# Performance work log

Hardware: AMD Instinct MI355X
Metric: run time of the kernel (lower is better)

## Reference

```python
import jax, jax.numpy as jnp
import numpy as np

B, N1, N2, H, LAT, MID = 16, 2048, 2048, 768, 128, 256


def setup_inputs() -> dict:
    key = jax.random.key(0)
    ks = jax.random.split(key, 20)
    def lin(k, n_in, n_out):
        s = 1.0 / np.sqrt(n_in)
        kw, kb = jax.random.split(k)
        W = jax.random.uniform(kw, (n_in, n_out), jnp.float32, -s, s)
        b = jax.random.uniform(kb, (n_out,), jnp.float32, -s, s)
        return W, b
    We1, be1 = lin(ks[0], H, MID)
    We2, be2 = lin(ks[1], MID, LAT)
    Wq, bq = lin(ks[2], LAT, LAT)
    Wk, bk = lin(ks[3], LAT, LAT)
    Wv, bv = lin(ks[4], LAT, LAT)
    Wd1, bd1 = lin(ks[5], LAT, MID)
    Wd2, bd2 = lin(ks[6], MID, H)
    main_feature = jax.random.normal(ks[7], (B, N1, H), jnp.float32)
    feature = jax.random.normal(ks[8], (B, N2, H), jnp.float32)
    return dict(main_feature=main_feature, feature=feature,
                We1=We1, be1=be1, We2=We2, be2=be2,
                Wq=Wq, bq=bq, Wk=Wk, bk=bk, Wv=Wv, bv=bv,
                Wd1=Wd1, bd1=bd1, Wd2=Wd2, bd2=bd2)


def reference(main_feature, feature, We1, be1, We2, be2, Wq, bq, Wk, bk, Wv, bv, Wd1, bd1, Wd2, bd2):
    def encode(x):
        h = jax.nn.relu(x @ We1 + be1)
        return jax.nn.relu(h @ We2 + be2)  # [B, N, LAT]

    def decode(x):
        h = jax.nn.relu(x @ Wd1 + bd1)
        return jax.nn.sigmoid(h @ Wd2 + bd2)  # [B, N, H]

    m = encode(main_feature)           # [B, N1, LAT]
    f = encode(feature)                # [B, N2, LAT]
    q = m @ Wq + bq                    # [B, N1, LAT]
    k = f @ Wk + bk                    # [B, N2, LAT]
    v = f @ Wv + bv                    # [B, N2, LAT]
    scores = jnp.einsum('bnd,bmd->bnm', q, k)   # unscaled, [B, N1, N2]
    probs = jax.nn.softmax(scores, axis=-1)
    attn = jnp.einsum('bnm,bmd->bnd', probs, v)  # [B, N1, LAT]
    return decode(attn)                # [B, N1, H]
```

## Files before the change

kernel.cpp:

```cpp
#include <hip/hip_runtime.h>
#include <stdint.h>

typedef unsigned short u16;
typedef __bf16 bf16x8 __attribute__((ext_vector_type(8)));
typedef float f32x4 __attribute__((ext_vector_type(4)));

#define MM   32768

__device__ __forceinline__ u16 f2bf(float f) {
    uint32_t u; __builtin_memcpy(&u, &f, 4);
    u += 0x7fffu + ((u >> 16) & 1u);
    return (u16)(u >> 16);
}

__device__ __forceinline__ void gl_lds16(const u16* g, u16* l) {
    __builtin_amdgcn_global_load_lds(
        (__attribute__((address_space(1))) void*)(g),
        (__attribute__((address_space(3))) void*)(l), 16, 0, 0);
}

__global__ void transpose_all(const float* __restrict__ We1, const float* __restrict__ We2,
                              const float* __restrict__ Wq,  const float* __restrict__ Wk,
                              const float* __restrict__ Wv,  const float* __restrict__ Wd1,
                              const float* __restrict__ Wd2, u16* __restrict__ wt) {
    int i = blockIdx.x * 256 + threadIdx.x;
    const float* src; int K, N, off;
    if      (i < 196608) { src = We1; K = 768; N = 256; off = i;          }
    else if (i < 229376) { src = We2; K = 256; N = 128; off = i - 196608; }
    else if (i < 245760) { src = Wq;  K = 128; N = 128; off = i - 229376; }
    else if (i < 262144) { src = Wk;  K = 128; N = 128; off = i - 245760; }
    else if (i < 278528) { src = Wv;  K = 128; N = 128; off = i - 262144; }
    else if (i < 311296) { src = Wd1; K = 128; N = 256; off = i - 278528; }
    else if (i < 507904) { src = Wd2; K = 256; N = 768; off = i - 311296; }
    else return;
    int n = off / K, k = off % K;
    wt[i] = f2bf(src[(size_t)k * N + n]);
}

template <int ACT, bool TRANS, bool A_F32, bool OUT_F32>
__global__ void gemm_bt(const void* __restrict__ Avp, const u16* __restrict__ Wt,
                        const float* __restrict__ bias, void* __restrict__ Cvp,
                        int M, int N, int K) {
    __shared__ u16 a_sh[128 * 64];
    __shared__ u16 b_sh[128 * 64];
    const int t = threadIdx.x;
    const int wave = t >> 6, lane = t & 63;
    const int lrow = lane & 15, quad = lane >> 4;
    const int wr = wave >> 1, wc = wave & 1;
    const int m0 = blockIdx.x * 128, n0 = blockIdx.y * 128;

    f32x4 acc[4][4];
#pragma unroll
    for (int i = 0; i < 4; i++)
#pragma unroll
        for (int j = 0; j < 4; j++) acc[i][j] = (f32x4){0.f, 0.f, 0.f, 0.f};

    for (int k0 = 0; k0 < K; k0 += 64) {
        if (A_F32) {
            const float* Af = (const float*)Avp;
#pragma unroll
            for (int it = 0; it < 8; it++) {
                int s = it * 256 + t;
                int row = s >> 4, kc = s & 15;
                float4 v = *(const float4*)(Af + (size_t)(m0 + row) * K + k0 + kc * 4);
                uint32_t p0 = (uint32_t)f2bf(v.x) | ((uint32_t)f2bf(v.y) << 16);
                uint32_t p1 = (uint32_t)f2bf(v.z) | ((uint32_t)f2bf(v.w) << 16);
                *(uint32_t*)&a_sh[row * 64 + kc * 4]     = p0;
                *(uint32_t*)&a_sh[row * 64 + kc * 4 + 2] = p1;
            }
        } else {
            const u16* Ab = (const u16*)Avp;
#pragma unroll
            for (int it = 0; it < 4; it++) {
                int s = it * 256 + t;
                gl_lds16(Ab + (size_t)(m0 + (s >> 3)) * K + k0 + (s & 7) * 8,
                         &a_sh[(it * 256 + wave * 64) * 8]);
            }
        }
#pragma unroll
        for (int it = 0; it < 4; it++) {
            int s = it * 256 + t;
            gl_lds16(Wt + (size_t)(n0 + (s >> 3)) * K + k0 + (s & 7) * 8,
                     &b_sh[(it * 256 + wave * 64) * 8]);
        }
        __syncthreads();
#pragma unroll
        for (int kk = 0; kk < 2; kk++) {
            bf16x8 af[4], bfv[4];
#pragma unroll
            for (int i = 0; i < 4; i++)
                af[i] = *(const bf16x8*)&a_sh[(wr * 64 + i * 16 + lrow) * 64 + kk * 32 + quad * 8];
#pragma unroll
            for (int j = 0; j < 4; j++)
                bfv[j] = *(const bf16x8*)&b_sh[(wc * 64 + j * 16 + lrow) * 64 + kk * 32 + quad * 8];
#pragma unroll
            for (int i = 0; i < 4; i++)
#pragma unroll
                for (int j = 0; j < 4; j++)
                    acc[i][j] = __builtin_amdgcn_mfma_f32_16x16x32_bf16(af[i], bfv[j], acc[i][j], 0, 0, 0);
        }
        __syncthreads();
    }

    float bv4[4];
#pragma unroll
    for (int j = 0; j < 4; j++) bv4[j] = bias[n0 + wc * 64 + j * 16 + lrow];

#pragma unroll
    for (int i = 0; i < 4; i++) {
#pragma unroll
        for (int j = 0; j < 4; j++) {
            const int col = n0 + wc * 64 + j * 16 + lrow;
            if (!TRANS) {
#pragma unroll
                for (int r = 0; r < 4; r++) {
                    float x = acc[i][j][r] + bv4[j];
                    if (ACT == 1) x = fmaxf(x, 0.f);
                    if (ACT == 2) x = 1.f / (1.f + __expf(-x));
                    const int row = m0 + wr * 64 + i * 16 + quad * 4 + r;
                    if (OUT_F32) ((float*)Cvp)[(size_t)row * N + col] = x;
                    else         ((u16*)Cvp)[(size_t)row * N + col] = f2bf(x);
                }
            } else {
                u16 vv[4];
#pragma unroll
                for (int r = 0; r < 4; r++) vv[r] = f2bf(acc[i][j][r] + bv4[j]);
                u16* Cb = (u16*)Cvp;
                size_t base = (size_t)(m0 >> 11) * ((size_t)N * 2048) + (size_t)col * 2048 +
                              (m0 & 2047) + wr * 64 + i * 16 + quad * 4;
                *(uint32_t*)&Cb[base]     = (uint32_t)vv[0] | ((uint32_t)vv[1] << 16);
                *(uint32_t*)&Cb[base + 2] = (uint32_t)vv[2] | ((uint32_t)vv[3] << 16);
            }
        }
    }
}

__global__ __launch_bounds__(256)
void flash_attn(const u16* __restrict__ Q, const u16* __restrict__ Kb,
                const u16* __restrict__ VT, u16* __restrict__ O) {
    __shared__ u16 k_sh[64 * 128];
    __shared__ u16 v_sh[128 * 64];
    __shared__ u16 qp_sh[64 * 128];

    const int t = threadIdx.x, wave = t >> 6, lane = t & 63;
    const int lrow = lane & 15, quad = lane >> 4;
    const int lsw = (lrow & 7) << 3;
    const int b = blockIdx.x >> 5, q0 = (blockIdx.x & 31) * 64;

    const u16* qg = Q + (size_t)(b * 2048 + q0) * 128;
#pragma unroll
    for (int it = 0; it < 4; it++) {
        int s = it * 256 + t;
        int srcSeg = s ^ ((s >> 4) & 7);
        gl_lds16(qg + (size_t)srcSeg * 8, &qp_sh[(it * 256 + wave * 64) * 8]);
    }
    __syncthreads();
    bf16x8 qf[4];
#pragma unroll
    for (int ks = 0; ks < 4; ks++)
        qf[ks] = *(const bf16x8*)&qp_sh[(((wave * 16 + lrow) * 128) + ks * 32 + quad * 8) ^ lsw];

    f32x4 o_acc[8];
#pragma unroll
    for (int ct = 0; ct < 8; ct++) o_acc[ct] = (f32x4){0.f, 0.f, 0.f, 0.f};
    float m_i[4] = {-1e30f, -1e30f, -1e30f, -1e30f};
    float l_i[4] = {0.f, 0.f, 0.f, 0.f};

    for (int tile = 0; tile < 32; tile++) {
        const u16* kg = Kb + (size_t)(b * 2048 + tile * 64) * 128;
        const u16* vg = VT + (size_t)b * 262144 + tile * 64;
#pragma unroll
        for (int it = 0; it < 4; it++) {
            int s = it * 256 + t;
            int srcSeg = s ^ ((s >> 4) & 7);
            gl_lds16(kg + (size_t)srcSeg * 8, &k_sh[(it * 256 + wave * 64) * 8]);
        }
#pragma unroll
        for (int it = 0; it < 4; it++) {
            int s = it * 256 + t;
            int row = s >> 3, c = (s & 7) ^ (row & 7);
            gl_lds16(vg + (size_t)row * 2048 + c * 8,
                     &v_sh[(it * 256 + wave * 64) * 8]);
        }
        __syncthreads();

        f32x4 s_acc[4];
        __builtin_amdgcn_s_setprio(1);
#pragma unroll
        for (int ct = 0; ct < 4; ct++) {
            f32x4 a = (f32x4){0.f, 0.f, 0.f, 0.f};
#pragma unroll
            for (int ks = 0; ks < 4; ks++) {
                bf16x8 kf = *(const bf16x8*)&k_sh[(((ct * 16 + lrow) * 128) + ks * 32 + quad * 8) ^ lsw];
                a = __builtin_amdgcn_mfma_f32_16x16x32_bf16(qf[ks], kf, a, 0, 0, 0);
            }
            s_acc[ct] = a;
        }
        __builtin_amdgcn_s_setprio(0);

        float mnew[4], alpha[4], ps[4];
#pragma unroll
        for (int r = 0; r < 4; r++) {
            float mx = s_acc[0][r];
#pragma unroll
            for (int ct = 1; ct < 4; ct++) mx = fmaxf(mx, s_acc[ct][r]);
#pragma unroll
            for (int d = 8; d >= 1; d >>= 1) mx = fmaxf(mx, __shfl_xor(mx, d, 64));
            mnew[r] = fmaxf(m_i[r], mx);
            alpha[r] = __expf(m_i[r] - mnew[r]);
            m_i[r] = mnew[r];
            ps[r] = 0.f;
        }
#pragma unroll
        for (int ct = 0; ct < 4; ct++)
#pragma unroll
            for (int r = 0; r < 4; r++) {
                float p = __expf(s_acc[ct][r] - mnew[r]);
                ps[r] += p;
                qp_sh[(((wave * 16 + quad * 4 + r) * 128) + ct * 16 + lrow) ^ (((quad * 4 + r) & 7) << 3)] = f2bf(p);
            }
#pragma unroll
        for (int r = 0; r < 4; r++) {
#pragma unroll
            for (int d = 8; d >= 1; d >>= 1) ps[r] += __shfl_xor(ps[r], d, 64);
            l_i[r] = l_i[r] * alpha[r] + ps[r];
        }
#pragma unroll
        for (int ct = 0; ct < 8; ct++)
#pragma unroll
            for (int r = 0; r < 4; r++) o_acc[ct][r] *= alpha[r];

        bf16x8 pf[2];
#pragma unroll
        for (int ks = 0; ks < 2; ks++)
            pf[ks] = *(const bf16x8*)&qp_sh[(((wave * 16 + lrow) * 128) + ks * 32 + quad * 8) ^ lsw];
        __builtin_amdgcn_s_setprio(1);
#pragma unroll
        for (int ct = 0; ct < 8; ct++)
#pragma unroll
            for (int ks = 0; ks < 2; ks++) {
                bf16x8 vf = *(const bf16x8*)&v_sh[(((ct * 16 + lrow) * 64) + ks * 32 + quad * 8) ^ lsw];
                o_acc[ct] = __builtin_amdgcn_mfma_f32_16x16x32_bf16(pf[ks], vf, o_acc[ct], 0, 0, 0);
            }
        __builtin_amdgcn_s_setprio(0);
        __syncthreads();
    }

    float inv_l[4];
#pragma unroll
    for (int r = 0; r < 4; r++) inv_l[r] = 1.f / l_i[r];
#pragma unroll
    for (int ct = 0; ct < 8; ct++)
#pragma unroll
        for (int r = 0; r < 4; r++) {
            const int row = b * 2048 + q0 + wave * 16 + quad * 4 + r;
            O[(size_t)row * 128 + ct * 16 + lrow] = f2bf(o_acc[ct][r] * inv_l[r]);
        }
}

extern "C" void kernel_launch(void* const* d_in, const int* in_sizes, int n_in,
                              void* d_out, int out_size, void* d_ws, size_t ws_size,
                              hipStream_t stream) {
    const float* mainf = (const float*)d_in[0];
    const float* feat  = (const float*)d_in[1];
    const float* We1 = (const float*)d_in[2];  const float* be1 = (const float*)d_in[3];
    const float* We2 = (const float*)d_in[4];  const float* be2 = (const float*)d_in[5];
    const float* Wq  = (const float*)d_in[6];  const float* bq  = (const float*)d_in[7];
    const float* Wk  = (const float*)d_in[8];  const float* bk  = (const float*)d_in[9];
    const float* Wv  = (const float*)d_in[10]; const float* bv  = (const float*)d_in[11];
    const float* Wd1 = (const float*)d_in[12]; const float* bd1 = (const float*)d_in[13];
    const float* Wd2 = (const float*)d_in[14]; const float* bd2 = (const float*)d_in[15];

    u16* ws = (u16*)d_ws;
    u16* wt = ws;
    u16* h1 = wt + 524288;
    u16* mf = h1 + 8388608;
    u16* qb = mf + 4194304;
    u16* kb = qb + 4194304;
    u16* vT = kb + 4194304;
    u16* wt_e1 = wt, *wt_e2 = wt + 196608, *wt_q = wt + 229376, *wt_k = wt + 245760,
       * wt_v = wt + 262144, *wt_d1 = wt + 278528, *wt_d2 = wt + 311296;

    transpose_all<<<1984, 256, 0, stream>>>(We1, We2, Wq, Wk, Wv, Wd1, Wd2, wt);

    gemm_bt<1, false, true,  false><<<dim3(256, 2), 256, 0, stream>>>(mainf, wt_e1, be1, h1, MM, 256, 768);
    gemm_bt<1, false, false, false><<<dim3(256, 1), 256, 0, stream>>>(h1,    wt_e2, be2, mf, MM, 128, 256);
    gemm_bt<0, false, false, false><<<dim3(256, 1), 256, 0, stream>>>(mf,    wt_q,  bq,  qb, MM, 128, 128);
    gemm_bt<1, false, true,  false><<<dim3(256, 2), 256, 0, stream>>>(feat, wt_e1, be1, h1, MM, 256, 768);
    gemm_bt<1, false, false, false><<<dim3(256, 1), 256, 0, stream>>>(h1,   wt_e2, be2, mf, MM, 128, 256);
    gemm_bt<0, false, false, false><<<dim3(256, 1), 256, 0, stream>>>(mf,   wt_k,  bk,  kb, MM, 128, 128);
    gemm_bt<0, true,  false, false><<<dim3(256, 1), 256, 0, stream>>>(mf,   wt_v,  bv,  vT, MM, 128, 128);

    flash_attn<<<512, 256, 0, stream>>>(qb, kb, vT, mf);

    gemm_bt<1, false, false, false><<<dim3(256, 2), 256, 0, stream>>>(mf, wt_d1, bd1, h1, MM, 256, 128);
    gemm_bt<2, false, false, true ><<<dim3(256, 6), 256, 0, stream>>>(h1, wt_d2, bd2, d_out, MM, 768, 256);
}
```

Measured before the change: 565.4 us.

## Double-buffer GEMM shared tiles and shrink M tile to 64 rows

The GEMM kernel gets double-buffered LDS tiles. The next K-slice is issued (direct-to-LDS for bf16, into registers for fp32 A) while MFMAs run on the current slice, which leaves one barrier per iteration. The M tile is now a template parameter and all launches use 64 rows, doubling the grid so more blocks run across the CUs. The trade-off is lower reuse of the B tile per block, twice the LDS footprint, and extra registers for the fp32 prefetch.

```diff
diff --git a/kernel.cpp b/kernel.cpp
--- a/kernel.cpp
+++ b/kernel.cpp
@@ -37,69 +37,96 @@
     wt[i] = f2bf(src[(size_t)k * N + n]);
 }
 
-template <int ACT, bool TRANS, bool A_F32, bool OUT_F32>
+template <int BM, int ACT, bool TRANS, bool A_F32, bool OUT_F32>
 __global__ void gemm_bt(const void* __restrict__ Avp, const u16* __restrict__ Wt,
                         const float* __restrict__ bias, void* __restrict__ Cvp,
                         int M, int N, int K) {
-    __shared__ u16 a_sh[128 * 64];
-    __shared__ u16 b_sh[128 * 64];
+    constexpr int MI  = BM / 32;
+    constexpr int AF4 = BM / 16;
+    __shared__ u16 a_sh[2][BM * 64];
+    __shared__ u16 b_sh[2][128 * 64];
     const int t = threadIdx.x;
     const int wave = t >> 6, lane = t & 63;
     const int lrow = lane & 15, quad = lane >> 4;
     const int wr = wave >> 1, wc = wave & 1;
-    const int m0 = blockIdx.x * 128, n0 = blockIdx.y * 128;
-
-    f32x4 acc[4][4];
-#pragma unroll
-    for (int i = 0; i < 4; i++)
+    const int m0 = blockIdx.x * BM, n0 = blockIdx.y * 128;
+
+    const float* Af = (const float*)Avp;
+    const u16*   Ab = (const u16*)Avp;
+
+    f32x4 acc[MI][4];
+#pragma unroll
+    for (int i = 0; i < MI; i++)
 #pragma unroll
         for (int j = 0; j < 4; j++) acc[i][j] = (f32x4){0.f, 0.f, 0.f, 0.f};
 
+    float4 pf[A_F32 ? AF4 : 1];
+
+    auto stage_b = [&](int buf, int k0) {
+#pragma unroll
+        for (int it = 0; it < 4; it++) {
+            int s = it * 256 + t;
+            gl_lds16(Wt + (size_t)(n0 + (s >> 3)) * K + k0 + (s & 7) * 8,
+                     &b_sh[buf][(it * 256 + wave * 64) * 8]);
+        }
+    };
+    auto stage_a_bf = [&](int buf, int k0) {
+#pragma unroll
+        for (int it = 0; it < BM / 32; it++) {
+            int s = it * 256 + t;
+            gl_lds16(Ab + (size_t)(m0 + (s >> 3)) * K + k0 + (s & 7) * 8,
+                     &a_sh[buf][(it * 256 + wave * 64) * 8]);
+        }
+    };
+    auto load_a_f32 = [&](int k0) {
+#pragma unroll
+        for (int it = 0; it < AF4; it++) {
+            int s = it * 256 + t;
+            pf[it] = *(const float4*)(Af + (size_t)(m0 + (s >> 4)) * K + k0 + (s & 15) * 4);
+        }
+    };
+    auto write_a_f32 = [&](int buf) {
+#pragma unroll
+        for (int it = 0; it < AF4; it++) {
+            int s = it * 256 + t;
+            int row = s >> 4, kc = s & 15;
+            float4 v = pf[it];
+            uint32_t p0 = (uint32_t)f2bf(v.x) | ((uint32_t)f2bf(v.y) << 16);
+            uint32_t p1 = (uint32_t)f2bf(v.z) | ((uint32_t)f2bf(v.w) << 16);
+            *(uint32_t*)&a_sh[buf][row * 64 + kc * 4]     = p0;
+            *(uint32_t*)&a_sh[buf][row * 64 + kc * 4 + 2] = p1;
+        }
+    };
+
+    if (A_F32) { load_a_f32(0); write_a_f32(0); } else stage_a_bf(0, 0);
+    stage_b(0, 0);
+    __syncthreads();
+
+    int cur = 0;
     for (int k0 = 0; k0 < K; k0 += 64) {
-        if (A_F32) {
-            const float* Af = (const float*)Avp;
-#pragma unroll
-            for (int it = 0; it < 8; it++) {
-                int s = it * 256 + t;
-                int row = s >> 4, kc = s & 15;
-                float4 v = *(const float4*)(Af + (size_t)(m0 + row) * K + k0 + kc * 4);
-                uint32_t p0 = (uint32_t)f2bf(v.x) | ((uint32_t)f2bf(v.y) << 16);
-                uint32_t p1 = (uint32_t)f2bf(v.z) | ((uint32_t)f2bf(v.w) << 16);
-                *(uint32_t*)&a_sh[row * 64 + kc * 4]     = p0;
-                *(uint32_t*)&a_sh[row * 64 + kc * 4 + 2] = p1;
-            }
-        } else {
-            const u16* Ab = (const u16*)Avp;
-#pragma unroll
-            for (int it = 0; it < 4; it++) {
-                int s = it * 256 + t;
-                gl_lds16(Ab + (size_t)(m0 + (s >> 3)) * K + k0 + (s & 7) * 8,
-                         &a_sh[(it * 256 + wave * 64) * 8]);
-            }
-        }
-#pragma unroll
-        for (int it = 0; it < 4; it++) {
-            int s = it * 256 + t;
-            gl_lds16(Wt + (size_t)(n0 + (s >> 3)) * K + k0 + (s & 7) * 8,
-                     &b_sh[(it * 256 + wave * 64) * 8]);
-        }
-        __syncthreads();
+        const int nk = k0 + 64;
+        if (nk < K) {
+            if (A_F32) load_a_f32(nk); else stage_a_bf(cur ^ 1, nk);
+            stage_b(cur ^ 1, nk);
+        }
 #pragma unroll
         for (int kk = 0; kk < 2; kk++) {
-            bf16x8 af[4], bfv[4];
-#pragma unroll
-            for (int i = 0; i < 4; i++)
-                af[i] = *(const bf16x8*)&a_sh[(wr * 64 + i * 16 + lrow) * 64 + kk * 32 + quad * 8];
+            bf16x8 af[MI], bfv[4];
+#pragma unroll
+            for (int i = 0; i < MI; i++)
+                af[i] = *(const bf16x8*)&a_sh[cur][(wr * (BM / 2) + i * 16 + lrow) * 64 + kk * 32 + quad * 8];
 #pragma unroll
             for (int j = 0; j < 4; j++)
-                bfv[j] = *(const bf16x8*)&b_sh[(wc * 64 + j * 16 + lrow) * 64 + kk * 32 + quad * 8];
-#pragma unroll
-            for (int i = 0; i < 4; i++)
+                bfv[j] = *(const bf16x8*)&b_sh[cur][(wc * 64 + j * 16 + lrow) * 64 + kk * 32 + quad * 8];
+#pragma unroll
+            for (int i = 0; i < MI; i++)
 #pragma unroll
                 for (int j = 0; j < 4; j++)
                     acc[i][j] = __builtin_amdgcn_mfma_f32_16x16x32_bf16(af[i], bfv[j], acc[i][j], 0, 0, 0);
         }
+        if (A_F32 && nk < K) write_a_f32(cur ^ 1);
         __syncthreads();
+        cur ^= 1;
     }
 
     float bv4[4];
@@ -107,7 +134,7 @@
     for (int j = 0; j < 4; j++) bv4[j] = bias[n0 + wc * 64 + j * 16 + lrow];
 
 #pragma unroll
-    for (int i = 0; i < 4; i++) {
+    for (int i = 0; i < MI; i++) {
 #pragma unroll
         for (int j = 0; j < 4; j++) {
             const int col = n0 + wc * 64 + j * 16 + lrow;
@@ -117,7 +144,7 @@
                     float x = acc[i][j][r] + bv4[j];
                     if (ACT == 1) x = fmaxf(x, 0.f);
                     if (ACT == 2) x = 1.f / (1.f + __expf(-x));
-                    const int row = m0 + wr * 64 + i * 16 + quad * 4 + r;
+                    const int row = m0 + wr * (BM / 2) + i * 16 + quad * 4 + r;
                     if (OUT_F32) ((float*)Cvp)[(size_t)row * N + col] = x;
                     else         ((u16*)Cvp)[(size_t)row * N + col] = f2bf(x);
                 }
@@ -127,7 +154,7 @@
                 for (int r = 0; r < 4; r++) vv[r] = f2bf(acc[i][j][r] + bv4[j]);
                 u16* Cb = (u16*)Cvp;
                 size_t base = (size_t)(m0 >> 11) * ((size_t)N * 2048) + (size_t)col * 2048 +
-                              (m0 & 2047) + wr * 64 + i * 16 + quad * 4;
+                              (m0 & 2047) + wr * (BM / 2) + i * 16 + quad * 4;
                 *(uint32_t*)&Cb[base]     = (uint32_t)vv[0] | ((uint32_t)vv[1] << 16);
                 *(uint32_t*)&Cb[base + 2] = (uint32_t)vv[2] | ((uint32_t)vv[3] << 16);
             }
@@ -283,16 +310,16 @@
 
     transpose_all<<<1984, 256, 0, stream>>>(We1, We2, Wq, Wk, Wv, Wd1, Wd2, wt);
 
-    gemm_bt<1, false, true,  false><<<dim3(256, 2), 256, 0, stream>>>(mainf, wt_e1, be1, h1, MM, 256, 768);
-    gemm_bt<1, false, false, false><<<dim3(256, 1), 256, 0, stream>>>(h1,    wt_e2, be2, mf, MM, 128, 256);
-    gemm_bt<0, false, false, false><<<dim3(256, 1), 256, 0, stream>>>(mf,    wt_q,  bq,  qb, MM, 128, 128);
-    gemm_bt<1, false, true,  false><<<dim3(256, 2), 256, 0, stream>>>(feat, wt_e1, be1, h1, MM, 256, 768);
-    gemm_bt<1, false, false, false><<<dim3(256, 1), 256, 0, stream>>>(h1,   wt_e2, be2, mf, MM, 128, 256);
-    gemm_bt<0, false, false, false><<<dim3(256, 1), 256, 0, stream>>>(mf,   wt_k,  bk,  kb, MM, 128, 128);
-    gemm_bt<0, true,  false, false><<<dim3(256, 1), 256, 0, stream>>>(mf,   wt_v,  bv,  vT, MM, 128, 128);
+    gemm_bt<64, 1, false, true,  false><<<dim3(512, 2), 256, 0, stream>>>(mainf, wt_e1, be1, h1, MM, 256, 768);
+    gemm_bt<64, 1, false, false, false><<<dim3(512, 1), 256, 0, stream>>>(h1,    wt_e2, be2, mf, MM, 128, 256);
+    gemm_bt<64, 0, false, false, false><<<dim3(512, 1), 256, 0, stream>>>(mf,    wt_q,  bq,  qb, MM, 128, 128);
+    gemm_bt<64, 1, false, true,  false><<<dim3(512, 2), 256, 0, stream>>>(feat, wt_e1, be1, h1, MM, 256, 768);
+    gemm_bt<64, 1, false, false, false><<<dim3(512, 1), 256, 0, stream>>>(h1,   wt_e2, be2, mf, MM, 128, 256);
+    gemm_bt<64, 0, false, false, false><<<dim3(512, 1), 256, 0, stream>>>(mf,   wt_k,  bk,  kb, MM, 128, 128);
+    gemm_bt<64, 0, true,  false, false><<<dim3(512, 1), 256, 0, stream>>>(mf,   wt_v,  bv,  vT, MM, 128, 128);
 
     flash_attn<<<512, 256, 0, stream>>>(qb, kb, vT, mf);
 
-    gemm_bt<1, false, false, false><<<dim3(256, 2), 256, 0, stream>>>(mf, wt_d1, bd1, h1, MM, 256, 128);
-    gemm_bt<2, false, false, true ><<<dim3(256, 6), 256, 0, stream>>>(h1, wt_d2, bd2, d_out, MM, 768, 256);
-}
+    gemm_bt<64, 1, false, false, false><<<dim3(512, 2), 256, 0, stream>>>(mf, wt_d1, bd1, h1, MM, 256, 128);
+    gemm_bt<64, 2, false, false, true ><<<dim3(512, 6), 256, 0, stream>>>(h1, wt_d2, bd2, d_out, MM, 768, 256);
+}
```

Result: faster. 496.1 us (-12.3%).
